# Kernel tuning notes

Measured on AMD Instinct MI355X. Metric: run time of the kernel, lower is better.

## Reference

```python
import jax, jax.numpy as jnp
import numpy as np

B, NP, FEAT, DEG, H = 16, 1024, 512, 16, 1024
E = B * NP * DEG
RATIO = 0.8


def setup_inputs() -> dict:
    key = jax.random.key(0)
    ks = jax.random.split(key, 16)
    x = jax.random.normal(ks[0], (B * NP, FEAT), jnp.float32)
    g = jnp.repeat(jnp.arange(B, dtype=jnp.int32), NP * DEG)
    src = jax.random.randint(ks[1], (E,), 0, NP, jnp.int32) + g * NP
    dst = jax.random.randint(ks[2], (E,), 0, NP, jnp.int32) + g * NP
    edge_index = jnp.stack([src, dst])
    batch = jnp.repeat(jnp.arange(B, dtype=jnp.int32), NP)
    sc = 0.02
    inp = dict(x=x, edge_index=edge_index, batch=batch)
    # SAGEConv params: out = lin_l(mean_agg) + lin_r(x); bias only on lin_l (PyG default)
    inp['W1l'] = sc * jax.random.normal(ks[3], (H, FEAT), jnp.float32)
    inp['b1'] = jnp.zeros((H,), jnp.float32)
    inp['W1r'] = sc * jax.random.normal(ks[4], (H, FEAT), jnp.float32)
    inp['p1'] = jax.random.normal(ks[5], (H,), jnp.float32)
    inp['W2l'] = sc * jax.random.normal(ks[6], (H, H), jnp.float32)
    inp['b2'] = jnp.zeros((H,), jnp.float32)
    inp['W2r'] = sc * jax.random.normal(ks[7], (H, H), jnp.float32)
    inp['p2'] = jax.random.normal(ks[8], (H,), jnp.float32)
    inp['W3l'] = sc * jax.random.normal(ks[9], (H, H), jnp.float32)
    inp['b3'] = jnp.zeros((H,), jnp.float32)
    inp['W3r'] = sc * jax.random.normal(ks[10], (H, H), jnp.float32)
    inp['p3'] = jax.random.normal(ks[11], (H,), jnp.float32)
    return inp


def _sage(x, src, dst, w, Wl, b, Wr, n_nodes):
    # mean aggregation over (masked) incoming edges, isolated nodes -> 0
    deg = jax.ops.segment_sum(w, dst, num_segments=n_nodes)
    agg = jax.ops.segment_sum(x[src] * w[:, None], dst, num_segments=n_nodes)
    mean = agg / jnp.maximum(deg, 1.0)[:, None]
    return mean @ Wl.T + b + x @ Wr.T


def _topk_pool(x, src, dst, mask, p, n_per):
    # PyG TopKPooling: score = tanh((x.w)/||w||); keep top ceil(ratio*n) per graph
    k = int(np.ceil(RATIO * n_per))
    s = jnp.tanh((x @ p) / jnp.linalg.norm(p))
    vals, idx = jax.lax.top_k(s.reshape(B, n_per), k)          # [B,k]
    old = (idx + (jnp.arange(B, dtype=idx.dtype) * n_per)[:, None]).reshape(-1)
    x_new = x[old] * vals.reshape(-1)[:, None]                  # gate kept nodes by score
    remap = jnp.full((B * n_per,), -1, jnp.int32).at[old].set(jnp.arange(B * k, dtype=jnp.int32))
    s2, d2 = remap[src], remap[dst]
    m2 = mask & (s2 >= 0) & (d2 >= 0)                           # drop edges losing an endpoint
    return x_new, jnp.where(m2, s2, 0), jnp.where(m2, d2, 0), m2, k


def _readout(x, n_per):
    xr = x.reshape(B, n_per, H)
    return jnp.concatenate([xr.max(axis=1), xr.mean(axis=1)], axis=1)  # [B, 2H]


def reference(x, edge_index, batch, W1l, b1, W1r, p1, W2l, b2, W2r, p2, W3l, b3, W3r, p3):
    src, dst = edge_index[0], edge_index[1]
    mask = jnp.ones((src.shape[0],), bool)
    n = NP
    h = jax.nn.relu(_sage(x, src, dst, mask.astype(x.dtype), W1l, b1, W1r, B * n))
    h, src, dst, mask, n = _topk_pool(h, src, dst, mask, p1, n)
    x1 = _readout(h, n)
    h = jax.nn.relu(_sage(h, src, dst, mask.astype(h.dtype), W2l, b2, W2r, B * n))
    h, src, dst, mask, n = _topk_pool(h, src, dst, mask, p2, n)
    x2 = _readout(h, n)
    h = jax.nn.relu(_sage(h, src, dst, mask.astype(h.dtype), W3l, b3, W3r, B * n))
    h, src, dst, mask, n = _topk_pool(h, src, dst, mask, p3, n)
    x3 = _readout(h, n)
    return x1 + x2 + x3
```

## Files before the change

### kernel.cpp

```cpp
#include <hip/hip_runtime.h>
#include <math.h>

#define B_    16
#define NP_   1024
#define FEAT_ 512
#define H_    1024
#define E_    262144
#define EPG_  16384
#define K1_   820
#define K2_   656
#define K3_   525
#define M1_   16384
#define M2_   13120
#define M3_   10496
#define MP1_  16384
#define MP2_  13312
#define MP3_  11264
#define SPROWS_ 16384

typedef unsigned short ushort_t;
typedef __bf16 bf16x8 __attribute__((ext_vector_type(8)));
typedef float f32x4 __attribute__((ext_vector_type(4)));

__device__ inline ushort_t f2bf(float f) {
    unsigned u = __float_as_uint(f);
    u += 0x7FFF + ((u >> 16) & 1);
    return (ushort_t)(u >> 16);
}
__device__ inline float bf2f(ushort_t h) {
    return __uint_as_float(((unsigned)h) << 16);
}
__device__ inline void split1(float v, ushort_t& hi, ushort_t& lo) {
    hi = f2bf(v);
    lo = f2bf(v - bf2f(hi));
}

__device__ inline void gll16(const void* g, void* l) {
    __builtin_amdgcn_global_load_lds((__attribute__((address_space(1))) void*)g,
                                     (__attribute__((address_space(3))) void*)l, 16, 0, 0);
}


__global__ __launch_bounds__(1024) void prep2_kernel(const int* __restrict__ ei,
                                                     int* __restrict__ counts,
                                                     int* __restrict__ offsets,
                                                     int* __restrict__ adj,
                                                     const float* __restrict__ p1,
                                                     const float* __restrict__ p2,
                                                     const float* __restrict__ p3,
                                                     float* __restrict__ pnout,
                                                     const float* __restrict__ W1l, const float* __restrict__ W1r,
                                                     const float* __restrict__ W2l, const float* __restrict__ W2r,
                                                     const float* __restrict__ W3l, const float* __restrict__ W3r,
                                                     ushort_t* __restrict__ Wb1, ushort_t* __restrict__ Wb2,
                                                     ushort_t* __restrict__ Wb3) {
    int t = threadIdx.x;
    if (blockIdx.x < 16) {
        __shared__ int cnt[1024];
        __shared__ int scanb[1024];
        int b = blockIdx.x;
        int e0 = b * EPG_;
        cnt[t] = 0;
        __syncthreads();
        for (int e = e0 + t; e < e0 + EPG_; e += 1024)
            atomicAdd(&cnt[ei[E_ + e] - b * NP_], 1);
        __syncthreads();
        int v = cnt[t];
        scanb[t] = v;
        __syncthreads();
        for (int off = 1; off < 1024; off <<= 1) {
            int tv = (t >= off) ? scanb[t - off] : 0;
            __syncthreads();
            scanb[t] += tv;
            __syncthreads();
        }
        int excl = scanb[t] - v;
        counts[b * NP_ + t] = v;
        offsets[b * NP_ + t] = e0 + excl;
        cnt[t] = excl;
        __syncthreads();
        for (int e = e0 + t; e < e0 + EPG_; e += 1024) {
            int s = ei[e];
            int dloc = ei[E_ + e] - b * NP_;
            int pos = atomicAdd(&cnt[dloc], 1);
            adj[e0 + pos] = s;
        }
        return;
    }
    if (blockIdx.x < 19) {
        const float* p = blockIdx.x == 16 ? p1 : (blockIdx.x == 17 ? p2 : p3);
        __shared__ float red[1024];
        float a = p[t];
        red[t] = a * a;
        __syncthreads();
        for (int s = 512; s > 0; s >>= 1) {
            if (t < s) red[t] += red[t + s];
            __syncthreads();
        }
        if (t == 0) pnout[blockIdx.x - 16] = sqrtf(red[0]);
        return;
    }
    int idx = (blockIdx.x - 19) * 1024 + t;
    if (idx >= 524288 + 1048576 + 1048576) return;
    const float *Wl, *Wr; ushort_t* Wbig; int K;
    if (idx < 524288) { Wl = W1l; Wr = W1r; Wbig = Wb1; K = 512; }
    else if (idx < 524288 + 1048576) { idx -= 524288; Wl = W2l; Wr = W2r; Wbig = Wb2; K = 1024; }
    else { idx -= 524288 + 1048576; Wl = W3l; Wr = W3r; Wbig = Wb3; K = 1024; }
    int n = idx / K;
    int k = idx - n * K;
    ushort_t* row = Wbig + (size_t)n * (4 * K);
    float a = Wl[idx];
    ushort_t ah = f2bf(a);
    row[k] = ah;
    row[K + k] = f2bf(a - bf2f(ah));
    float b = Wr[idx];
    ushort_t bh = f2bf(b);
    row[2 * K + k] = bh;
    row[3 * K + k] = f2bf(b - bf2f(bh));
}


__global__ __launch_bounds__(128) void agg1_k512(const float* __restrict__ x,
                                                 const int* __restrict__ adj,
                                                 const int* __restrict__ offsets,
                                                 const int* __restrict__ counts,
                                                 ushort_t* __restrict__ Abig) {
    int gid = blockIdx.x;
    int xcd = gid & 7;
    int u = gid >> 3;
    int half = u & 1;
    int pi = u >> 1;
    int gsel = (pi >= 512) ? 1 : 0;
    int g = xcd + (gsel << 3);
    int node = g * 1024 + (pi - (gsel << 9)) * 2 + (threadIdx.x >> 6);
    int c = threadIdx.x & 63;
    int col4 = half * 64 + c;
    int start = offsets[node], cnt = counts[node];
    float d = fmaxf((float)cnt, 1.0f);
    const float4* xb = (const float4*)x;
    float ax = 0.f, ay = 0.f, az = 0.f, aw = 0.f;
    int j = 0;
    for (; j + 8 <= cnt; j += 8) {
        int si[8];
#pragma unroll
        for (int q = 0; q < 8; ++q) si[q] = adj[start + j + q];
        float4 vv[8];
#pragma unroll
        for (int q = 0; q < 8; ++q) vv[q] = xb[(size_t)si[q] * 128 + col4];
#pragma unroll
        for (int q = 0; q < 8; ++q) {
            ax += vv[q].x; ay += vv[q].y; az += vv[q].z; aw += vv[q].w;
        }
    }
    for (; j + 4 <= cnt; j += 4) {
        int s0 = adj[start + j + 0], s1 = adj[start + j + 1];
        int s2 = adj[start + j + 2], s3 = adj[start + j + 3];
        float4 v0 = xb[(size_t)s0 * 128 + col4];
        float4 v1 = xb[(size_t)s1 * 128 + col4];
        float4 v2 = xb[(size_t)s2 * 128 + col4];
        float4 v3 = xb[(size_t)s3 * 128 + col4];
        ax += (v0.x + v1.x) + (v2.x + v3.x);
        ay += (v0.y + v1.y) + (v2.y + v3.y);
        az += (v0.z + v1.z) + (v2.z + v3.z);
        aw += (v0.w + v1.w) + (v2.w + v3.w);
    }
    for (; j < cnt; ++j) {
        float4 v = xb[(size_t)adj[start + j] * 128 + col4];
        ax += v.x; ay += v.y; az += v.z; aw += v.w;
    }
    float inv = 1.0f / d;
    float4 cv = xb[(size_t)node * 128 + col4];
    ushort_t* row = Abig + (size_t)node * 2048;
    int f = col4 * 4;
    ushort4 mh, ml, ch, cl;
    split1(ax * inv, mh.x, ml.x); split1(ay * inv, mh.y, ml.y);
    split1(az * inv, mh.z, ml.z); split1(aw * inv, mh.w, ml.w);
    split1(cv.x, ch.x, cl.x); split1(cv.y, ch.y, cl.y);
    split1(cv.z, ch.z, cl.z); split1(cv.w, ch.w, cl.w);
    *(ushort4*)&row[f]        = mh;
    *(ushort4*)&row[512 + f]  = ml;
    *(ushort4*)&row[1024 + f] = ch;
    *(ushort4*)&row[1536 + f] = cl;
}

template<int LAYER>
__global__ __launch_bounds__(128) void agg23_k1024(const float* __restrict__ h,
                                                   const int* __restrict__ adj,
                                                   const int* __restrict__ offsets,
                                                   const int* __restrict__ counts,
                                                   const int* __restrict__ old_idx,
                                                   const float* __restrict__ vals,
                                                   ushort_t* __restrict__ Abig,
                                                   int n_per, int M, int npad) {
    int gid = blockIdx.x;
    if (gid >= 32 * n_per) {
        int r = gid - 32 * n_per;
        if (r < npad) {
            uint4* row = (uint4*)(Abig + (size_t)(M + r) * 4096);
#pragma unroll
            for (int q = 0; q < 4; ++q) row[threadIdx.x + q * 128] = (uint4){0, 0, 0, 0};
        }
        return;
    }
    int xcd = gid & 7;
    int u = gid >> 3;
    int half = u & 1;
    int nl = u >> 1;
    int gsel = (nl >= n_per) ? 1 : 0;
    int g = xcd + (gsel << 3);
    int node = g * n_per + nl - gsel * n_per;
    int c = threadIdx.x;
    int col4 = half * 128 + c;
    int start = offsets[node], cnt = counts[node];
    float d = fmaxf((float)cnt, 1.0f);
    const float4* hb = (const float4*)h;
    float ax = 0.f, ay = 0.f, az = 0.f, aw = 0.f;
    int j = 0;
    for (; j + 8 <= cnt; j += 8) {
        int si[8];
#pragma unroll
        for (int q = 0; q < 8; ++q) si[q] = adj[start + j + q];
        int oi[8]; float wi[8];
#pragma unroll
        for (int q = 0; q < 8; ++q) { oi[q] = old_idx[si[q]]; wi[q] = vals[si[q]]; }
        float4 vv[8];
#pragma unroll
        for (int q = 0; q < 8; ++q) vv[q] = hb[(size_t)oi[q] * 256 + col4];
#pragma unroll
        for (int q = 0; q < 8; ++q) {
            ax += wi[q] * vv[q].x; ay += wi[q] * vv[q].y;
            az += wi[q] * vv[q].z; aw += wi[q] * vv[q].w;
        }
    }
    for (; j + 4 <= cnt; j += 4) {
        int s0 = adj[start + j + 0], s1 = adj[start + j + 1];
        int s2 = adj[start + j + 2], s3 = adj[start + j + 3];
        int o0 = old_idx[s0], o1 = old_idx[s1], o2 = old_idx[s2], o3 = old_idx[s3];
        float w0 = vals[s0], w1 = vals[s1], w2 = vals[s2], w3 = vals[s3];
        float4 v0 = hb[(size_t)o0 * 256 + col4];
        float4 v1 = hb[(size_t)o1 * 256 + col4];
        float4 v2 = hb[(size_t)o2 * 256 + col4];
        float4 v3 = hb[(size_t)o3 * 256 + col4];
        ax += (w0 * v0.x + w1 * v1.x) + (w2 * v2.x + w3 * v3.x);
        ay += (w0 * v0.y + w1 * v1.y) + (w2 * v2.y + w3 * v3.y);
        az += (w0 * v0.z + w1 * v1.z) + (w2 * v2.z + w3 * v3.z);
        aw += (w0 * v0.w + w1 * v1.w) + (w2 * v2.w + w3 * v3.w);
    }
    for (; j < cnt; ++j) {
        int s = adj[start + j];
        int o = old_idx[s];
        float w = vals[s];
        float4 v = hb[(size_t)o * 256 + col4];
        ax += w * v.x; ay += w * v.y; az += w * v.z; aw += w * v.w;
    }
    float inv = 1.0f / d;
    int on = old_idx[node];
    float vn = vals[node];
    float4 cv = hb[(size_t)on * 256 + col4];
    cv.x *= vn; cv.y *= vn; cv.z *= vn; cv.w *= vn;
    ushort_t* row = Abig + (size_t)node * 4096;
    int f = col4 * 4;
    ushort4 mh, ml, ch, cl;
    split1(ax * inv, mh.x, ml.x); split1(ay * inv, mh.y, ml.y);
    split1(az * inv, mh.z, ml.z); split1(aw * inv, mh.w, ml.w);
    split1(cv.x, ch.x, cl.x); split1(cv.y, ch.y, cl.y);
    split1(cv.z, ch.z, cl.z); split1(cv.w, ch.w, cl.w);
    *(ushort4*)&row[f]        = mh;
    *(ushort4*)&row[1024 + f] = ml;
    *(ushort4*)&row[2048 + f] = ch;
    *(ushort4*)&row[3072 + f] = cl;
}


#define STR_(x) #x
#define VMW2_(n) asm volatile("s_waitcnt vmcnt(" STR_(n) ")" ::: "memory")
#define VMW(n) VMW2_(n)
#define BARM() do { __builtin_amdgcn_s_barrier(); asm volatile("" ::: "memory"); } while (0)

#define STG(Lw_, pl_, src_, c_) {                                                   \
    const ushort_t* s_ = (src_) + (c_);                                             \
    gll16(s_, (Lw_) + (pl_) * 8192);                                                \
    gll16(s_ + rstep, (Lw_) + (pl_) * 8192 + 4096);                                 \
}

#define MFQ(I0, Aarr, A0, Barr)                                                     \
    _Pragma("unroll")                                                               \
    for (int ii = 0; ii < 4; ++ii) {                                                \
        _Pragma("unroll")                                                           \
        for (int jj = 0; jj < 4; ++jj)                                              \
            acc[(I0) + ii][jj] = __builtin_amdgcn_mfma_f32_16x16x32_bf16(           \
                Aarr[(A0) + ii], Barr[jj], acc[(I0) + ii][jj], 0, 0, 0);            \
    }

#define CHUNK(t_, b_, stg_, pre_, XA, XB, YA, YB) do {                              \
    int cs_ = ((t_) + 1 < NC2) ? ((t_) + 1) * 32 : 2 * KK + ((t_) + 1 - NC2) * 32;  \
    const ushort_t* Lr = L + (b_) * 32768;                                          \
    const ushort_t* Lq = L + (1 - (b_)) * 32768;                                    \
    ushort_t* Lw = L + (1 - (b_)) * 32768 + tid * 8;                                \
    bf16x8 al[8], bl[4];                                                            \
    _Pragma("unroll") for (int q = 0; q < 8; ++q)                                   \
        al[q] = *(const bf16x8*)&Lr[8192 + aoff + q * 512];                         \
    _Pragma("unroll") for (int q = 0; q < 4; ++q)                                   \
        bl[q] = *(const bf16x8*)&Lr[24576 + boff + q * 512];                        \
    if (stg_) {                                                                     \
        STG(Lw, 0, Ag, cs_);                                                        \
        STG(Lw, 2, Bg, cs_);                                                        \
        STG(Lw, 1, Ag + KK, cs_);                                                   \
        STG(Lw, 3, Bg + KK, cs_);                                                   \
    }                                                                               \
    __builtin_amdgcn_s_setprio(1);                                                  \
    MFQ(0, XA, 0, XB);                                                              \
    MFQ(4, XA, 4, XB);                                                              \
    MFQ(0, al, 0, XB);                                                              \
    MFQ(4, al, 4, XB);                                                              \
    __builtin_amdgcn_s_setprio(0);                                                  \
    VMW(0);                                                                         \
    BARM();                                                                         \
    if (pre_) {                                                                     \
        _Pragma("unroll") for (int q = 0; q < 8; ++q)                               \
            YA[q] = *(const bf16x8*)&Lq[aoff + q * 512];                            \
        _Pragma("unroll") for (int q = 0; q < 4; ++q)                               \
            YB[q] = *(const bf16x8*)&Lq[16384 + boff + q * 512];                    \
    }                                                                               \
    __builtin_amdgcn_s_setprio(1);                                                  \
    MFQ(0, XA, 0, bl);                                                              \
    MFQ(4, XA, 4, bl);                                                              \
    __builtin_amdgcn_s_setprio(0);                                                  \
} while (0)

template<int KK>
__global__ __launch_bounds__(512, 2) void gemm256(const ushort_t* __restrict__ Ab,
                                                  const ushort_t* __restrict__ Wb,
                                                  const float* __restrict__ bias,
                                                  float* __restrict__ C,
                                                  float* __restrict__ sp,
                                                  const float* __restrict__ pvec,
                                                  int npanels) {
    constexpr int LD  = 4 * KK;
    constexpr int NC  = KK / 16;
    constexpr int NC2 = KK / 32;
    __shared__ ushort_t L[65536];

    int tid = threadIdx.x;
    int lane = tid & 63;
    int w = tid >> 6;
    int wm = w >> 2, wn = w & 3;

    int nb = npanels * 4;
    int per = nb >> 3;
    int bp = (blockIdx.x & 7) * per + (blockIdx.x >> 3);
    int panel = bp >> 2, cb = bp & 3;
    int m0 = panel * 256, n0 = cb * 256;

    int srow = tid >> 2;
    int gq = (tid & 3) ^ (srow & 3) ^ ((srow >> 2) & 3);
    const ushort_t* Ag = Ab + (size_t)(m0 + srow) * LD + gq * 8;
    const ushort_t* Bg = Wb + (size_t)(n0 + srow) * LD + gq * 8;
    const size_t rstep = (size_t)128 * LD;

    int qsw = (lane >> 4) ^ (lane & 3) ^ ((lane >> 2) & 3);
    int aoff = (wm * 128 + (lane & 15)) * 32 + qsw * 8;
    int boff = (wn * 64 + (lane & 15)) * 32 + qsw * 8;

    f32x4 acc[8][4];
#pragma unroll
    for (int i = 0; i < 8; ++i)
#pragma unroll
        for (int j = 0; j < 4; ++j) acc[i][j] = (f32x4){0.f, 0.f, 0.f, 0.f};

    bf16x8 ahA[8], bhA[4], ahB[8], bhB[4];

    {
        ushort_t* Lw0 = L + tid * 8;
        STG(Lw0, 0, Ag, 0);
        STG(Lw0, 2, Bg, 0);
        STG(Lw0, 1, Ag + KK, 0);
        STG(Lw0, 3, Bg + KK, 0);
        VMW(0);
        BARM();
#pragma unroll
        for (int q = 0; q < 8; ++q) ahA[q] = *(const bf16x8*)&L[aoff + q * 512];
#pragma unroll
        for (int q = 0; q < 4; ++q) bhA[q] = *(const bf16x8*)&L[16384 + boff + q * 512];
    }

#pragma unroll 1
    for (int t = 0; t < NC - 2; t += 2) {
        CHUNK(t,     0, 1, 1, ahA, bhA, ahB, bhB);
        CHUNK(t + 1, 1, 1, 1, ahB, bhB, ahA, bhA);
    }
    CHUNK(NC - 2, 0, 1, 1, ahA, bhA, ahB, bhB);
    CHUNK(NC - 1, 1, 0, 0, ahB, bhB, ahA, bhA);

    float bj[4], pj[4];
#pragma unroll
    for (int j = 0; j < 4; ++j) {
        int col = n0 + wn * 64 + j * 16 + (lane & 15);
        bj[j] = bias[col];
        pj[j] = pvec[col];
    }
    int slot = cb * 4 + wn;
#pragma unroll
    for (int i = 0; i < 8; ++i) {
        int row0 = m0 + wm * 128 + i * 16 + (lane >> 4) * 4;
        float sacc[4] = {0.f, 0.f, 0.f, 0.f};
#pragma unroll
        for (int j = 0; j < 4; ++j) {
            int col = n0 + wn * 64 + j * 16 + (lane & 15);
#pragma unroll
            for (int r = 0; r < 4; ++r) {
                float v = acc[i][j][r] + bj[j];
                v = v > 0.f ? v : 0.f;
                C[(size_t)(row0 + r) * 1024 + col] = v;
                sacc[r] += v * pj[j];
            }
        }
#pragma unroll
        for (int r = 0; r < 4; ++r) {
            float sv_ = sacc[r];
            sv_ += __shfl_xor(sv_, 1);
            sv_ += __shfl_xor(sv_, 2);
            sv_ += __shfl_xor(sv_, 4);
            sv_ += __shfl_xor(sv_, 8);
            if ((lane & 15) == 0) sp[slot * SPROWS_ + row0 + r] = sv_;
        }
    }
}


template<int FIRST>
__global__ __launch_bounds__(1024) void tail_kernel(const float* __restrict__ sp,
                                                    const float* __restrict__ pn,
                                                    const float* __restrict__ h,
                                                    float* __restrict__ out,
                                                    int n, int k,
                                                    int* __restrict__ old_idx, float* __restrict__ vals,
                                                    const int* __restrict__ ei,
                                                    int* __restrict__ esrc, int* __restrict__ edst,
                                                    int* __restrict__ emask,
                                                    int* __restrict__ counts, int* __restrict__ offsets,
                                                    int* __restrict__ adj, int do_edges) {
    __shared__ float sv[1024];
    __shared__ int   rmap[1024];
    __shared__ int   oi_s[1024];
    __shared__ float vv_s[1024];
    __shared__ float4 rmx[32][32];
    __shared__ float4 rsm[32][32];
    int b = blockIdx.x / 9, role = blockIdx.x % 9;
    int t = threadIdx.x;
    if (role == 8 && !do_edges) return;

    float mine = -INFINITY;
    if (t < n) {
        int base = b * n + t;
        float s0 = 0.f;
#pragma unroll
        for (int c = 0; c < 16; ++c) s0 += sp[c * SPROWS_ + base];
        mine = s0;
    }
    sv[t] = mine;
    __syncthreads();
    int rank = 0;
#pragma unroll 4
    for (int j = 0; j < 1024; ++j) {
        float o = sv[j];
        rank += (o > mine) || (o == mine && j < t);
    }
    bool kept = (t < n) && (rank < k);
    rmap[t] = kept ? rank : -1;
    if (kept) {
        float tv = tanhf(mine / pn[0]);
        oi_s[rank] = b * n + t;
        vv_s[rank] = tv;
        if (role == 8) {
            old_idx[b * k + rank] = b * n + t;
            vals[b * k + rank] = tv;
        }
    }
    __syncthreads();

    if (role < 8) {
        int c32 = t & 31, g = t >> 5;
        int col4 = role * 32 + c32;
        const float4* hb = (const float4*)h;
        float4 mx = {-INFINITY, -INFINITY, -INFINITY, -INFINITY};
        float4 sm = {0.f, 0.f, 0.f, 0.f};
        for (int i = g; i < k; i += 32) {
            int o = oi_s[i];
            float wgt = vv_s[i];
            float4 v = hb[(size_t)o * 256 + col4];
            v.x *= wgt; v.y *= wgt; v.z *= wgt; v.w *= wgt;
            mx.x = fmaxf(mx.x, v.x); mx.y = fmaxf(mx.y, v.y);
            mx.z = fmaxf(mx.z, v.z); mx.w = fmaxf(mx.w, v.w);
            sm.x += v.x; sm.y += v.y; sm.z += v.z; sm.w += v.w;
        }
        rmx[g][c32] = mx; rsm[g][c32] = sm;
        __syncthreads();
        for (int s = 16; s > 0; s >>= 1) {
            if (g < s) {
                float4 om = rmx[g + s][c32], os = rsm[g + s][c32];
                float4 m = rmx[g][c32], ss2 = rsm[g][c32];
                m.x = fmaxf(m.x, om.x); m.y = fmaxf(m.y, om.y);
                m.z = fmaxf(m.z, om.z); m.w = fmaxf(m.w, om.w);
                ss2.x += os.x; ss2.y += os.y; ss2.z += os.z; ss2.w += os.w;
                rmx[g][c32] = m; rsm[g][c32] = ss2;
            }
            __syncthreads();
        }
        if (g == 0) {
            float4 m = rmx[0][c32], ss2 = rsm[0][c32];
            float invk = 1.0f / (float)k;
            float* o0 = out + (size_t)b * 2048 + col4 * 4;
            float* o1 = o0 + 1024;
            if (FIRST) {
                o0[0] = m.x; o0[1] = m.y; o0[2] = m.z; o0[3] = m.w;
                o1[0] = ss2.x * invk; o1[1] = ss2.y * invk;
                o1[2] = ss2.z * invk; o1[3] = ss2.w * invk;
            } else {
                o0[0] += m.x; o0[1] += m.y; o0[2] += m.z; o0[3] += m.w;
                o1[0] += ss2.x * invk; o1[1] += ss2.y * invk;
                o1[2] += ss2.z * invk; o1[3] += ss2.w * invk;
            }
        }
        return;
    }

    __shared__ int cnt_s[1024];
    cnt_s[t] = 0;
    __syncthreads();
    int e0 = b * EPG_;
    for (int e = e0 + t; e < e0 + EPG_; e += 1024) {
        int ms = FIRST ? 1 : emask[e];
        if (ms) {
            int s = FIRST ? ei[e] : esrc[e];
            int dd = FIRST ? ei[E_ + e] : edst[e];
            int ns = rmap[s - b * n];
            int nd = rmap[dd - b * n];
            if (ns >= 0 && nd >= 0) atomicAdd(&cnt_s[nd], 1);
        }
    }
    __syncthreads();
    int v = (t < k) ? cnt_s[t] : 0;
    oi_s[t] = v;
    __syncthreads();
    for (int off = 1; off < 1024; off <<= 1) {
        int tv = (t >= off) ? oi_s[t - off] : 0;
        __syncthreads();
        oi_s[t] += tv;
        __syncthreads();
    }
    int excl = oi_s[t] - v;
    if (t < k) {
        counts[b * k + t] = v;
        offsets[b * k + t] = e0 + excl;
        cnt_s[t] = excl;
    }
    __syncthreads();
    for (int e = e0 + t; e < e0 + EPG_; e += 1024) {
        int ms = FIRST ? 1 : emask[e];
        if (ms) {
            int s = FIRST ? ei[e] : esrc[e];
            int dd = FIRST ? ei[E_ + e] : edst[e];
            int ns = rmap[s - b * n];
            int nd = rmap[dd - b * n];
            if (ns >= 0 && nd >= 0) {
                int gs = b * k + ns;
                esrc[e] = gs;
                edst[e] = b * k + nd;
                if (FIRST) emask[e] = 1;
                int pos = atomicAdd(&cnt_s[nd], 1);
                adj[e0 + pos] = gs;
            } else {
                emask[e] = 0;
            }
        } else if (FIRST) {
            emask[e] = 0;
        }
    }
}


extern "C" void kernel_launch(void* const* d_in, const int* in_sizes, int n_in,
                              void* d_out, int out_size, void* d_ws, size_t ws_size,
                              hipStream_t stream) {
    const float* x   = (const float*)d_in[0];
    const int*   ei  = (const int*)d_in[1];
    const float* W1l = (const float*)d_in[3];
    const float* b1  = (const float*)d_in[4];
    const float* W1r = (const float*)d_in[5];
    const float* p1  = (const float*)d_in[6];
    const float* W2l = (const float*)d_in[7];
    const float* b2  = (const float*)d_in[8];
    const float* W2r = (const float*)d_in[9];
    const float* p2  = (const float*)d_in[10];
    const float* W3l = (const float*)d_in[11];
    const float* b3  = (const float*)d_in[12];
    const float* W3r = (const float*)d_in[13];
    const float* p3  = (const float*)d_in[14];
    float* out = (float*)d_out;

    char* ws = (char*)d_ws;
    size_t off = 0;
    float* bufOut = (float*)(ws + off); off += (size_t)MP1_ * 1024 * 4;
    ushort_t* Abig = (ushort_t*)(ws + off); off += (size_t)MP2_ * 4096 * 2;
    ushort_t* Wb1 = (ushort_t*)(ws + off); off += (size_t)1024 * 2048 * 2;
    ushort_t* Wb2 = (ushort_t*)(ws + off); off += (size_t)1024 * 4096 * 2;
    ushort_t* Wb3 = (ushort_t*)(ws + off); off += (size_t)1024 * 4096 * 2;
    float* sp = (float*)(ws + off); off += (size_t)16 * SPROWS_ * 4;
    char* misc = ws + off;
    int*   counts = (int*)(misc + 0 * 65536);
    int*   offsets= (int*)(misc + 1 * 65536);
    int*   old_idx= (int*)(misc + 2 * 65536);
    float* vals   = (float*)(misc + 3 * 65536);
    float* pnormv = (float*)(misc + 4 * 65536);
    int*   adj    = (int*)(misc + 5 * 65536);
    int*   esrc   = (int*)(misc + 5 * 65536 + 1 * 1048576);
    int*   edst   = (int*)(misc + 5 * 65536 + 2 * 1048576);
    int*   emask  = (int*)(misc + 5 * 65536 + 3 * 1048576);

    prep2_kernel<<<19 + (524288 + 2 * 1048576) / 1024, 1024, 0, stream>>>(
        ei, counts, offsets, adj, p1, p2, p3, pnormv,
        W1l, W1r, W2l, W2r, W3l, W3r, Wb1, Wb2, Wb3);

    agg1_k512<<<16384, 128, 0, stream>>>(x, adj, offsets, counts, Abig);
    gemm256<512><<<(MP1_ / 256) * 4, 512, 0, stream>>>(Abig, Wb1, b1, bufOut, sp, p1, MP1_ / 256);
    tail_kernel<1><<<B_ * 9, 1024, 0, stream>>>(sp, pnormv + 0, bufOut, out, NP_, K1_,
                                                old_idx, vals, ei, esrc, edst, emask,
                                                counts, offsets, adj, 1);

    agg23_k1024<2><<<32 * K1_ + (MP2_ - M2_), 128, 0, stream>>>(
        bufOut, adj, offsets, counts, old_idx, vals, Abig, K1_, M2_, MP2_ - M2_);
    gemm256<1024><<<(MP2_ / 256) * 4, 512, 0, stream>>>(Abig, Wb2, b2, bufOut, sp, p2, MP2_ / 256);
    tail_kernel<0><<<B_ * 9, 1024, 0, stream>>>(sp, pnormv + 1, bufOut, out, K1_, K2_,
                                                old_idx, vals, ei, esrc, edst, emask,
                                                counts, offsets, adj, 1);

    agg23_k1024<3><<<32 * K2_ + (MP3_ - M3_), 128, 0, stream>>>(
        bufOut, adj, offsets, counts, old_idx, vals, Abig, K2_, M3_, MP3_ - M3_);
    gemm256<1024><<<(MP3_ / 256) * 4, 512, 0, stream>>>(Abig, Wb3, b3, bufOut, sp, p3, MP3_ / 256);
    tail_kernel<0><<<B_ * 9, 1024, 0, stream>>>(sp, pnormv + 2, bufOut, out, K2_, K3_,
                                                old_idx, vals, ei, esrc, edst, emask,
                                                counts, offsets, adj, 0);
}
```

Before: 747.9 us.

## Pre-tile A and W operands into LDS-ready blocks for contiguous GEMM staging

The aggregation kernels and the weight-prep kernel now write the split bf16 hi/lo operands in a tiled layout (per 256-row panel and 16-column chunk) that matches the GEMM's shared-memory layout. The GEMM then stages each chunk with contiguous 16-byte global-to-LDS loads and reads fragments with simple lane-linear offsets, with no XOR swizzle or row-strided addressing. This removes strided global reads and swizzle arithmetic from the GEMM loop. In exchange the producer kernels do scattered ushort4 and scalar stores. The LDS reads may also become more prone to bank conflicts without the swizzle.

```diff
diff --git a/kernel.cpp b/kernel.cpp
--- a/kernel.cpp
+++ b/kernel.cpp
@@ -17,6 +17,7 @@
 #define MP2_  13312
 #define MP3_  11264
 #define SPROWS_ 16384
+
 
 typedef unsigned short ushort_t;
 typedef __bf16 bf16x8 __attribute__((ext_vector_type(8)));
@@ -108,15 +109,21 @@
     else { idx -= 524288 + 1048576; Wl = W3l; Wr = W3r; Wbig = Wb3; K = 1024; }
     int n = idx / K;
     int k = idx - n * K;
-    ushort_t* row = Wbig + (size_t)n * (4 * K);
+    int p = n >> 8, prow = n & 255;
+    int S = ((prow >> 4) << 6) | (((k >> 3) & 3) << 4) | (prow & 15);
+    int NCk = K >> 4;
+    int tW = k >> 5;
+    int e = k & 7;
+    size_t bl_ = ((size_t)(p * NCk + tW)) * 16384 + S * 8 + e;
+    size_t br_ = ((size_t)(p * NCk + (NCk >> 1) + tW)) * 16384 + S * 8 + e;
     float a = Wl[idx];
     ushort_t ah = f2bf(a);
-    row[k] = ah;
-    row[K + k] = f2bf(a - bf2f(ah));
+    Wbig[bl_] = ah;
+    Wbig[bl_ + 8192] = f2bf(a - bf2f(ah));
     float b = Wr[idx];
     ushort_t bh = f2bf(b);
-    row[2 * K + k] = bh;
-    row[3 * K + k] = f2bf(b - bf2f(bh));
+    Wbig[br_] = bh;
+    Wbig[br_ + 8192] = f2bf(b - bf2f(bh));
 }
 
 
@@ -170,17 +177,20 @@
     }
     float inv = 1.0f / d;
     float4 cv = xb[(size_t)node * 128 + col4];
-    ushort_t* row = Abig + (size_t)node * 2048;
-    int f = col4 * 4;
     ushort4 mh, ml, ch, cl;
     split1(ax * inv, mh.x, ml.x); split1(ay * inv, mh.y, ml.y);
     split1(az * inv, mh.z, ml.z); split1(aw * inv, mh.w, ml.w);
     split1(cv.x, ch.x, cl.x); split1(cv.y, ch.y, cl.y);
     split1(cv.z, ch.z, cl.z); split1(cv.w, ch.w, cl.w);
-    *(ushort4*)&row[f]        = mh;
-    *(ushort4*)&row[512 + f]  = ml;
-    *(ushort4*)&row[1024 + f] = ch;
-    *(ushort4*)&row[1536 + f] = cl;
+    int p = node >> 8, prow = node & 255;
+    int S = ((prow >> 4) << 6) | (((col4 >> 1) & 3) << 4) | (prow & 15);
+    int e = (col4 & 1) * 4;
+    size_t ba = ((size_t)(p * 32 + (col4 >> 3))) * 16384 + S * 8 + e;
+    size_t bc = ((size_t)(p * 32 + 16 + (col4 >> 3))) * 16384 + S * 8 + e;
+    *(ushort4*)&Abig[ba]        = mh;
+    *(ushort4*)&Abig[ba + 8192] = ml;
+    *(ushort4*)&Abig[bc]        = ch;
+    *(ushort4*)&Abig[bc + 8192] = cl;
 }
 
 template<int LAYER>
@@ -196,9 +206,20 @@
     if (gid >= 32 * n_per) {
         int r = gid - 32 * n_per;
         if (r < npad) {
-            uint4* row = (uint4*)(Abig + (size_t)(M + r) * 4096);
-#pragma unroll
-            for (int q = 0; q < 4; ++q) row[threadIdx.x + q * 128] = (uint4){0, 0, 0, 0};
+            int row = M + r;
+            int p = row >> 8, prow = row & 255;
+            int rg6 = (prow >> 4) << 6, ri = prow & 15;
+            ushort4 z = {0, 0, 0, 0};
+            for (int cc = threadIdx.x; cc < 256; cc += 128) {
+                int S = rg6 | (((cc >> 1) & 3) << 4) | ri;
+                int e = (cc & 1) * 4;
+                size_t ba = ((size_t)(p * 64 + (cc >> 3))) * 16384 + S * 8 + e;
+                size_t bc = ((size_t)(p * 64 + 32 + (cc >> 3))) * 16384 + S * 8 + e;
+                *(ushort4*)&Abig[ba]        = z;
+                *(ushort4*)&Abig[ba + 8192] = z;
+                *(ushort4*)&Abig[bc]        = z;
+                *(ushort4*)&Abig[bc + 8192] = z;
+            }
         }
         return;
     }
@@ -258,17 +279,20 @@
     float vn = vals[node];
     float4 cv = hb[(size_t)on * 256 + col4];
     cv.x *= vn; cv.y *= vn; cv.z *= vn; cv.w *= vn;
-    ushort_t* row = Abig + (size_t)node * 4096;
-    int f = col4 * 4;
     ushort4 mh, ml, ch, cl;
     split1(ax * inv, mh.x, ml.x); split1(ay * inv, mh.y, ml.y);
     split1(az * inv, mh.z, ml.z); split1(aw * inv, mh.w, ml.w);
     split1(cv.x, ch.x, cl.x); split1(cv.y, ch.y, cl.y);
     split1(cv.z, ch.z, cl.z); split1(cv.w, ch.w, cl.w);
-    *(ushort4*)&row[f]        = mh;
-    *(ushort4*)&row[1024 + f] = ml;
-    *(ushort4*)&row[2048 + f] = ch;
-    *(ushort4*)&row[3072 + f] = cl;
+    int p = node >> 8, prow = node & 255;
+    int S = ((prow >> 4) << 6) | (((col4 >> 1) & 3) << 4) | (prow & 15);
+    int e = (col4 & 1) * 4;
+    size_t ba = ((size_t)(p * 64 + (col4 >> 3))) * 16384 + S * 8 + e;
+    size_t bc = ((size_t)(p * 64 + 32 + (col4 >> 3))) * 16384 + S * 8 + e;
+    *(ushort4*)&Abig[ba]        = mh;
+    *(ushort4*)&Abig[ba + 8192] = ml;
+    *(ushort4*)&Abig[bc]        = ch;
+    *(ushort4*)&Abig[bc + 8192] = cl;
 }
 
 
@@ -277,11 +301,18 @@
 #define VMW(n) VMW2_(n)
 #define BARM() do { __builtin_amdgcn_s_barrier(); asm volatile("" ::: "memory"); } while (0)
 
-#define STG(Lw_, pl_, src_, c_) {                                                   \
-    const ushort_t* s_ = (src_) + (c_);                                             \
-    gll16(s_, (Lw_) + (pl_) * 8192);                                                \
-    gll16(s_ + rstep, (Lw_) + (pl_) * 8192 + 4096);                                 \
-}
+#define STG8(Lw_, t_) do {                                                          \
+    size_t ab_ = ((size_t)(pA * NC + (t_))) * 16384;                                \
+    size_t bb_ = ((size_t)(cb * NC + (t_))) * 16384;                                \
+    gll16(Ab + ab_ + tid8,         (Lw_) + tid8);                                   \
+    gll16(Ab + ab_ + 4096 + tid8,  (Lw_) + 4096 + tid8);                            \
+    gll16(Ab + ab_ + 8192 + tid8,  (Lw_) + 8192 + tid8);                            \
+    gll16(Ab + ab_ + 12288 + tid8, (Lw_) + 12288 + tid8);                           \
+    gll16(Wb + bb_ + tid8,         (Lw_) + 16384 + tid8);                           \
+    gll16(Wb + bb_ + 4096 + tid8,  (Lw_) + 20480 + tid8);                           \
+    gll16(Wb + bb_ + 8192 + tid8,  (Lw_) + 24576 + tid8);                           \
+    gll16(Wb + bb_ + 12288 + tid8, (Lw_) + 28672 + tid8);                           \
+} while (0)
 
 #define MFQ(I0, Aarr, A0, Barr)                                                     \
     _Pragma("unroll")                                                               \
@@ -293,21 +324,15 @@
     }
 
 #define CHUNK(t_, b_, stg_, pre_, XA, XB, YA, YB) do {                              \
-    int cs_ = ((t_) + 1 < NC2) ? ((t_) + 1) * 32 : 2 * KK + ((t_) + 1 - NC2) * 32;  \
     const ushort_t* Lr = L + (b_) * 32768;                                          \
     const ushort_t* Lq = L + (1 - (b_)) * 32768;                                    \
-    ushort_t* Lw = L + (1 - (b_)) * 32768 + tid * 8;                                \
+    ushort_t* Lw = L + (1 - (b_)) * 32768;                                          \
     bf16x8 al[8], bl[4];                                                            \
     _Pragma("unroll") for (int q = 0; q < 8; ++q)                                   \
-        al[q] = *(const bf16x8*)&Lr[8192 + aoff + q * 512];                         \
+        al[q] = *(const bf16x8*)&Lr[8192 + wm * 4096 + q * 512 + ln8];              \
     _Pragma("unroll") for (int q = 0; q < 4; ++q)                                   \
-        bl[q] = *(const bf16x8*)&Lr[24576 + boff + q * 512];                        \
-    if (stg_) {                                                                     \
-        STG(Lw, 0, Ag, cs_);                                                        \
-        STG(Lw, 2, Bg, cs_);                                                        \
-        STG(Lw, 1, Ag + KK, cs_);                                                   \
-        STG(Lw, 3, Bg + KK, cs_);                                                   \
-    }                                                                               \
+        bl[q] = *(const bf16x8*)&Lr[24576 + wn * 2048 + q * 512 + ln8];             \
+    if (stg_) { STG8(Lw, (t_) + 1); }                                               \
     __builtin_amdgcn_s_setprio(1);                                                  \
     MFQ(0, XA, 0, XB);                                                              \
     MFQ(4, XA, 4, XB);                                                              \
@@ -318,9 +343,9 @@
     BARM();                                                                         \
     if (pre_) {                                                                     \
         _Pragma("unroll") for (int q = 0; q < 8; ++q)                               \
-            YA[q] = *(const bf16x8*)&Lq[aoff + q * 512];                            \
+            YA[q] = *(const bf16x8*)&Lq[wm * 4096 + q * 512 + ln8];                 \
         _Pragma("unroll") for (int q = 0; q < 4; ++q)                               \
-            YB[q] = *(const bf16x8*)&Lq[16384 + boff + q * 512];                    \
+            YB[q] = *(const bf16x8*)&Lq[16384 + wn * 2048 + q * 512 + ln8];         \
     }                                                                               \
     __builtin_amdgcn_s_setprio(1);                                                  \
     MFQ(0, XA, 0, bl);                                                              \
@@ -336,31 +361,21 @@
                                                   float* __restrict__ sp,
                                                   const float* __restrict__ pvec,
                                                   int npanels) {
-    constexpr int LD  = 4 * KK;
     constexpr int NC  = KK / 16;
-    constexpr int NC2 = KK / 32;
     __shared__ ushort_t L[65536];
 
     int tid = threadIdx.x;
     int lane = tid & 63;
+    int ln8 = lane * 8;
+    size_t tid8 = (size_t)tid * 8;
     int w = tid >> 6;
     int wm = w >> 2, wn = w & 3;
 
     int nb = npanels * 4;
     int per = nb >> 3;
     int bp = (blockIdx.x & 7) * per + (blockIdx.x >> 3);
-    int panel = bp >> 2, cb = bp & 3;
-    int m0 = panel * 256, n0 = cb * 256;
-
-    int srow = tid >> 2;
-    int gq = (tid & 3) ^ (srow & 3) ^ ((srow >> 2) & 3);
-    const ushort_t* Ag = Ab + (size_t)(m0 + srow) * LD + gq * 8;
-    const ushort_t* Bg = Wb + (size_t)(n0 + srow) * LD + gq * 8;
-    const size_t rstep = (size_t)128 * LD;
-
-    int qsw = (lane >> 4) ^ (lane & 3) ^ ((lane >> 2) & 3);
-    int aoff = (wm * 128 + (lane & 15)) * 32 + qsw * 8;
-    int boff = (wn * 64 + (lane & 15)) * 32 + qsw * 8;
+    int pA = bp >> 2, cb = bp & 3;
+    int m0 = pA * 256, n0 = cb * 256;
 
     f32x4 acc[8][4];
 #pragma unroll
@@ -371,17 +386,13 @@
     bf16x8 ahA[8], bhA[4], ahB[8], bhB[4];
 
     {
-        ushort_t* Lw0 = L + tid * 8;
-        STG(Lw0, 0, Ag, 0);
-        STG(Lw0, 2, Bg, 0);
-        STG(Lw0, 1, Ag + KK, 0);
-        STG(Lw0, 3, Bg + KK, 0);
+        STG8(L, 0);
         VMW(0);
         BARM();
 #pragma unroll
-        for (int q = 0; q < 8; ++q) ahA[q] = *(const bf16x8*)&L[aoff + q * 512];
-#pragma unroll
-        for (int q = 0; q < 4; ++q) bhA[q] = *(const bf16x8*)&L[16384 + boff + q * 512];
+        for (int q = 0; q < 8; ++q) ahA[q] = *(const bf16x8*)&L[wm * 4096 + q * 512 + ln8];
+#pragma unroll
+        for (int q = 0; q < 4; ++q) bhA[q] = *(const bf16x8*)&L[16384 + wn * 2048 + q * 512 + ln8];
     }
 
 #pragma unroll 1
```

Measured after the change: 947.9 us. 26.7% more time.
